# Optimization experiments

Measured on AMD Instinct MI355X. Metric: run time of the kernel, lower is better.

Reference implementation:

```python
import jax, jax.numpy as jnp
import numpy as np

NQ, NT, BSZ, E, NH = 100, 197, 128, 768, 12
HD = E // NH
EPS = 1e-12  # torch F.normalize default eps


def _l2norm(x, axis=-1):
    n = jnp.linalg.norm(x, axis=axis, keepdims=True)
    return x / jnp.maximum(n, EPS)


def setup_inputs() -> dict:
    rng = jax.random.key(0)
    ks = jax.random.split(rng, 10)
    s = 0.02  # xavier-ish scale for weights
    return {
        "query": jax.random.normal(ks[0], (NQ, BSZ, E), jnp.float32),
        "key": jax.random.normal(ks[1], (NT, BSZ, E), jnp.float32),
        "value": jax.random.normal(ks[2], (NT, BSZ, E), jnp.float32),
        "in_proj_weight": jax.random.normal(ks[3], (3 * E, E), jnp.float32) * s,
        "in_proj_bias": jnp.zeros((3 * E,), jnp.float32),
        "out_proj_weight": jax.random.normal(ks[4], (E, E), jnp.float32) * s,
        "out_proj_bias": jnp.zeros((E,), jnp.float32),
        "temperature": jnp.ones((NH, 1, 1), jnp.float32),
        "q_mapper": jax.random.normal(ks[5], (1, NT, NQ), jnp.float32),
        "x_mapper": jax.random.normal(ks[6], (1, NQ, NT), jnp.float32),
    }


def reference(query, key, value, in_proj_weight, in_proj_bias,
              out_proj_weight, out_proj_bias, temperature, q_mapper, x_mapper):
    nq, bsz, e = query.shape
    nt = key.shape[0]
    # packed in-projection: split into q/k/v weights
    wq, wk, wv = jnp.split(in_proj_weight, 3, axis=0)
    bq, bk, bv = jnp.split(in_proj_bias, 3, axis=0)
    q = query @ wq.T + bq   # [Nq, bsz, E]
    k = key @ wk.T + bk     # [Nt, bsz, E]
    v = value @ wv.T + bv   # [Nt, bsz, E]
    # reshape to [bsz, nh, hd, N] (channel-major for cross-covariance attn)
    q = q.reshape(nq, bsz, NH, HD).transpose(1, 2, 3, 0)  # [b, h, d, Nq]
    k = k.reshape(nt, bsz, NH, HD).transpose(1, 2, 3, 0)  # [b, h, d, Nt]
    v = v.reshape(nt, bsz, NH, HD).transpose(1, 2, 3, 0)  # [b, h, d, Nt]
    # normalize channel vectors over tokens
    qn = _l2norm(q)
    kn = _l2norm(k)
    # mappers: normalize over last dim, then shape to [Nq, Nt] operators
    qm_op = _l2norm(q_mapper[0])  # [Nt, Nq] normalized over Nq; transpose below
    xm_op = _l2norm(x_mapper[0])  # [Nq, Nt] normalized over Nt
    # qm = q @ q_mapper^T : [b,h,d,Nq] x [Nq,Nt] -> [b,h,d,Nt]
    qm = jnp.einsum('bhdq,tq->bhdt', qn, qm_op)
    # cross-covariance attention over channels: [b,h,d,d]
    attn = jnp.einsum('bhdt,bhet->bhde', qm, kn) * temperature[None]  # temp [nh,1,1] broadcasts per-head
    attn = jax.nn.softmax(attn, axis=-1)
    x = jnp.einsum('bhde,bhet->bhdt', attn, v)        # [b,h,d,Nt]
    out = jnp.einsum('bhdt,qt->bhdq', x, xm_op)       # [b,h,d,Nq]
    # back to [Nq, bsz, E]
    out = out.transpose(3, 0, 1, 2).reshape(nq, bsz, e)
    out = out @ out_proj_weight.T + out_proj_bias
    return out
```

## Files before the change

kernel.cpp:

```cpp
#include <hip/hip_runtime.h>
#include <hip/hip_bf16.h>

using bf16 = __hip_bfloat16;

constexpr int NQ  = 100;
constexpr int NT  = 197;
constexpr int BSZ = 128;
constexpr int EMB = 768;
constexpr int NHD = 12;
constexpr int HDD = 64;
constexpr int COLS = BSZ * EMB;
constexpr int M_Q  = 12800;
constexpr int M_KV = 25216;
constexpr int M_KVP = 25344;
constexpr int TPAD = 224;

constexpr size_t SZ_Q16  = (size_t)M_Q  * EMB * 2;
constexpr size_t SZ_KV16 = (size_t)M_KV * EMB * 2;
constexpr size_t SZ_KVP  = (size_t)M_KVP * EMB * 2;
constexpr size_t SZ_WI   = (size_t)3 * EMB * EMB * 2;
constexpr size_t SZ_T16  = (size_t)COLS * TPAD * 2;
constexpr size_t OFF_QB   = 256;
constexpr size_t OFF_KB   = OFF_QB + SZ_Q16;
constexpr size_t OFF_VB   = OFF_KB + SZ_KV16;
constexpr size_t OFF_WI   = OFF_VB + SZ_KV16;
constexpr size_t OFF_QP16 = OFF_WI + SZ_WI;
constexpr size_t OFF_KP16 = OFF_QP16 + SZ_Q16;
constexpr size_t OFF_VP16 = OFF_KP16 + SZ_KVP;
constexpr size_t OFF_QMNT = OFF_VP16 + SZ_KVP;
constexpr size_t OFF_XMNT = OFF_QMNT + 57344;
constexpr size_t OFF_WO   = OFF_XMNT + 57344;
constexpr size_t OFF_KPT  = 256;
constexpr size_t OFF_VPT  = OFF_KPT + SZ_T16;
constexpr size_t OFF_W16T = OFF_VPT + SZ_T16;
constexpr size_t OFF_QNT  = OFF_KP16;
constexpr size_t OFF_G16  = OFF_VP16;
constexpr size_t OFF_XO   = 256;

__device__ __forceinline__ float dl(const float* p) { return *p; }
__device__ __forceinline__ float dl(const bf16* p) { return __bfloat162float(*p); }

__device__ __forceinline__ ushort f2bf(float x) {
    union { float f; unsigned u; } v; v.f = x;
    unsigned r = v.u + 0x7FFFu + ((v.u >> 16) & 1u);
    return (ushort)(r >> 16);
}
__device__ __forceinline__ float bf2f(ushort x) {
    union { unsigned u; float f; } v; v.u = (unsigned)x << 16;
    return v.f;
}
__device__ __forceinline__ void dstore(float* p, float v) { *p = v; }
__device__ __forceinline__ void dstore(bf16* p, float v) { *p = __float2bfloat16(v); }

typedef __attribute__((ext_vector_type(8))) short short8;
typedef __attribute__((ext_vector_type(4))) short shortv4;
typedef __attribute__((ext_vector_type(4))) float f32x4;

__device__ __forceinline__ void gload16(const bf16* g, ushort* l) {
    __builtin_amdgcn_global_load_lds(
        (const __attribute__((address_space(1))) unsigned int*)g,
        (__attribute__((address_space(3))) unsigned int*)l, 16, 0, 0);
}

__device__ __forceinline__ int2 xcd_swz(int bx, int by, int gx, int gy) {
    const int nwg = gx * gy;
    const int L = by * gx + bx;
    const int q = nwg >> 3, r = nwg & 7;
    const int c = L & 7, i = L >> 3;
    const int wg = (c < r ? c * (q + 1) : r * (q + 1) + (c - r) * q) + i;
    return make_int2(wg % gx, wg / gx);
}

__global__ __launch_bounds__(256) void k_cvt5(
        const float* __restrict__ s0, bf16* __restrict__ d0,
        const float* __restrict__ s1, bf16* __restrict__ d1,
        const float* __restrict__ s2, bf16* __restrict__ d2,
        const float* __restrict__ s3, bf16* __restrict__ d3,
        const float* __restrict__ s4, bf16* __restrict__ d4) {
    int bk = blockIdx.x;
    const float* s; bf16* d; int lb;
    if      (bk < 864)   { s = s0; d = d0; lb = bk; }
    else if (bk < 5664)  { s = s1; d = d1; lb = bk - 864; }
    else if (bk < 15120) { s = s2; d = d2; lb = bk - 5664; }
    else if (bk < 24576) { s = s3; d = d3; lb = bk - 15120; }
    else                 { s = s4; d = d4; lb = bk - 24576; }
    size_t i = ((size_t)lb * 256 + threadIdx.x) * 8;
    float4 a = *(const float4*)(s + i), b = *(const float4*)(s + i + 4);
    short8 r;
    r[0] = (short)f2bf(a.x); r[1] = (short)f2bf(a.y); r[2] = (short)f2bf(a.z); r[3] = (short)f2bf(a.w);
    r[4] = (short)f2bf(b.x); r[5] = (short)f2bf(b.y); r[6] = (short)f2bf(b.z); r[7] = (short)f2bf(b.w);
    *(short8*)(d + i) = r;
}

template <typename T>
__global__ __launch_bounds__(256) void k_maps(const T* __restrict__ qm, bf16* qmnT,
                                              const T* __restrict__ xm, bf16* xmnT) {
    __shared__ float red[256];
    const int bk = blockIdx.x, tid = threadIdx.x;
    if (bk < 224) {
        int t = bk;
        float v = (t < NT && tid < NQ) ? dl(&qm[t * NQ + tid]) : 0.f;
        if (tid < 128) red[tid] = v * v;
        __syncthreads();
        for (int s = 64; s > 0; s >>= 1) { if (tid < s) red[tid] += red[tid + s]; __syncthreads(); }
        float inv = 1.f / fmaxf(sqrtf(red[0]), 1e-12f);
        if (tid < 128)
            dstore(&qmnT[(size_t)tid * TPAD + t], (t < NT && tid < NQ) ? v * inv : 0.f);
    } else {
        int q = bk - 224, t = tid;
        float v = (q < NQ && t < NT) ? dl(&xm[q * NT + t]) : 0.f;
        red[t] = v * v;
        __syncthreads();
        for (int s = 128; s > 0; s >>= 1) { if (t < s) red[t] += red[t + s]; __syncthreads(); }
        float inv = 1.f / fmaxf(sqrtf(red[0]), 1e-12f);
        if (t < TPAD) dstore(&xmnT[(size_t)q * TPAD + t], (q < NQ && t < NT) ? v * inv : 0.f);
    }
}

template <int NR, int TP, int NORM>
__global__ __launch_bounds__(256) void k_trn(const bf16* __restrict__ src,
        bf16* __restrict__ dst) {
    __shared__ ushort tile[TP * 73];
    __shared__ float ssp[4][64];
    __shared__ float inv_s[64];
    const int col0 = blockIdx.x * 64;
    const int tid = threadIdx.x;
    const int c = tid & 63, tb = tid >> 6;
    float ss = 0.f;
#pragma unroll
    for (int it = 0; it < TP / 4; ++it) {
        int t = tb + it * 4;
        ushort v = 0;
        if (t < NR) v = *(const ushort*)&src[(size_t)t * COLS + col0 + c];
        tile[t * 73 + c] = v;
        if (NORM) { float f = bf2f(v); ss = fmaf(f, f, ss); }
    }
    if (NORM) {
        ssp[tb][c] = ss;
        __syncthreads();
        if (tid < 64) {
            float s = ssp[0][tid] + ssp[1][tid] + ssp[2][tid] + ssp[3][tid];
            inv_s[tid] = 1.f / fmaxf(sqrtf(s), 1e-12f);
        }
    }
    __syncthreads();
    constexpr int UPC = TP / 8;
#pragma unroll
    for (int it = 0; it < (64 * UPC) / 256; ++it) {
        int u = tid + it * 256;
        int cc = u / UPC, t0 = (u % UPC) * 8;
        float inv = NORM ? inv_s[cc] : 1.f;
        short8 s;
#pragma unroll
        for (int r = 0; r < 8; ++r) {
            ushort raw = tile[(t0 + r) * 73 + cc];
            s[r] = NORM ? (short)f2bf(bf2f(raw) * inv) : (short)raw;
        }
        *(short8*)&dst[(size_t)(col0 + cc) * TP + t0] = s;
    }
}

__global__ __launch_bounds__(256) void k_trn2(const bf16* __restrict__ kp,
        const bf16* __restrict__ vp, bf16* __restrict__ kpT, bf16* __restrict__ vpT) {
    __shared__ ushort tile[TPAD * 73];
    __shared__ float ssp[4][64];
    __shared__ float inv_s[64];
    const int bk = blockIdx.x;
    const bool vseg = bk >= 1536;
    const bf16* src = vseg ? vp : kp;
    bf16* dst = vseg ? vpT : kpT;
    const int col0 = (vseg ? bk - 1536 : bk) * 64;
    const int tid = threadIdx.x;
    const int c = tid & 63, tb = tid >> 6;
    float ss = 0.f;
#pragma unroll
    for (int it = 0; it < TPAD / 4; ++it) {
        int t = tb + it * 4;
        ushort v = 0;
        if (t < NT) v = *(const ushort*)&src[(size_t)t * COLS + col0 + c];
        tile[t * 73 + c] = v;
        if (!vseg) { float f = bf2f(v); ss = fmaf(f, f, ss); }
    }
    if (!vseg) {
        ssp[tb][c] = ss;
        __syncthreads();
        if (tid < 64) {
            float s = ssp[0][tid] + ssp[1][tid] + ssp[2][tid] + ssp[3][tid];
            inv_s[tid] = 1.f / fmaxf(sqrtf(s), 1e-12f);
        }
    }
    __syncthreads();
    constexpr int UPC = TPAD / 8;
#pragma unroll
    for (int it = 0; it < (64 * UPC) / 256; ++it) {
        int u = tid + it * 256;
        int cc = u / UPC, t0 = (u % UPC) * 8;
        float inv = vseg ? 1.f : inv_s[cc];
        short8 s;
#pragma unroll
        for (int r = 0; r < 8; ++r) {
            ushort raw = tile[(t0 + r) * 73 + cc];
            s[r] = vseg ? (short)raw : (short)f2bf(bf2f(raw) * inv);
        }
        *(short8*)&dst[(size_t)(col0 + cc) * TPAD + t0] = s;
    }
}

#define MM8_BAR  { __builtin_amdgcn_s_barrier(); __builtin_amdgcn_sched_barrier(0); }
#define MM8_LGK0 { asm volatile("s_waitcnt lgkmcnt(0)" ::: "memory"); __builtin_amdgcn_sched_barrier(0); }
#define MM8_VM8  { asm volatile("s_waitcnt vmcnt(8)" ::: "memory"); __builtin_amdgcn_sched_barrier(0); }
#define MM8_VM0  { asm volatile("s_waitcnt vmcnt(0)" ::: "memory"); __builtin_amdgcn_sched_barrier(0); }
#define MM8_STAGE(CUR, ISB, H, KT) do { \
    const bf16* gb_ = (ISB) ? (Wb + (size_t)(n0 + (H)*128 + srow) * EMB + (KT)*64 + sk_sw) \
                            : (Ab + (size_t)(m0 + (H)*128 + srow) * EMB + (KT)*64 + sk_sw); \
    ushort* lb_ = ((ISB) ? B_lds : A_lds) + (CUR)*16384 + (H)*8192 + wid*512; \
    gload16(gb_, lb_); \
    gload16(gb_ + (size_t)64 * EMB, lb_ + 4096); \
} while (0)
#define MM8_LOADFRAGS(CUR, KK, AARR, BARR) { \
    _Pragma("unroll") for (int m_ = 0; m_ < 8; ++m_) { \
        int ra_ = wr*128 + m_*16 + ln15; \
        AARR[m_] = *(const short8*)&A_lds[(CUR)*16384 + ra_*64 + ((((KK)*4 + q8) ^ (ra_ & 7)))*8]; } \
    _Pragma("unroll") for (int j_ = 0; j_ < 4; ++j_) { \
        int rb_ = wc*64 + j_*16 + ln15; \
        BARR[j_] = *(const short8*)&B_lds[(CUR)*16384 + rb_*64 + ((((KK)*4 + q8) ^ (rb_ & 7)))*8]; } }
#define MM8_QUAD(AARR, BARR, MB) { \
    __builtin_amdgcn_s_setprio(1); \
    _Pragma("unroll") for (int m_ = 0; m_ < 4; ++m_) \
        _Pragma("unroll") for (int j_ = 0; j_ < 4; ++j_) \
            acc[(MB) + m_][j_] = __builtin_amdgcn_mfma_f32_16x16x32_bf16( \
                AARR[(MB) + m_], BARR[j_], acc[(MB) + m_][j_], 0, 0, 0); \
    __builtin_amdgcn_s_setprio(0); }

__global__ __launch_bounds__(512, 2) void k_mm8(
        const bf16* __restrict__ A0, const bf16* __restrict__ A1, const bf16* __restrict__ A2,
        const bf16* __restrict__ W,
        bf16* __restrict__ C0, bf16* __restrict__ C1, bf16* __restrict__ C2,
        const float* __restrict__ bias, int mt0, int mt01) {
    __shared__ __align__(16) ushort A_lds[2 * 16384];
    __shared__ __align__(16) ushort B_lds[2 * 16384];
    const int tid = threadIdx.x;
    const int2 bxy = xcd_swz(blockIdx.x, blockIdx.y, gridDim.x, gridDim.y);
    int seg = 0, lby = bxy.y;
    if (bxy.y < mt0)       { seg = 0; lby = bxy.y; }
    else if (bxy.y < mt01) { seg = 1; lby = bxy.y - mt0; }
    else                   { seg = 2; lby = bxy.y - mt01; }
    const bf16* Ab = seg == 0 ? A0 : (seg == 1 ? A1 : A2);
    const bf16* Wb = W + (size_t)seg * EMB * EMB;
    bf16* C = seg == 0 ? C0 : (seg == 1 ? C1 : C2);
    const float* bp = bias + seg * EMB;
    const int m0 = lby * 256, n0 = bxy.x * 256;
    const int wid = tid >> 6, ln = tid & 63;
    const int wr = wid >> 2, wc = wid & 3;
    const int ln15 = ln & 15, q8 = ln >> 4;
    const int srow = tid >> 3;
    const int sk_sw = (((tid & 7) ^ (srow & 7)) * 8);

    f32x4 acc[8][4] = {};
    short8 a0[8], b0[4], a1[8], b1[4];

    MM8_STAGE(0, 0, 0, 0); MM8_STAGE(0, 0, 1, 0); MM8_STAGE(0, 1, 0, 0); MM8_STAGE(0, 1, 1, 0);
    MM8_STAGE(1, 0, 0, 1); MM8_STAGE(1, 0, 1, 1); MM8_STAGE(1, 1, 0, 1); MM8_STAGE(1, 1, 1, 1);
    MM8_VM8;
    MM8_BAR;

    for (int t = 0; t < 12; ++t) {
        const int c = t & 1, nxt = t + 2;
        MM8_LOADFRAGS(c, 0, a0, b0);
        MM8_QUAD(a0, b0, 0);
        MM8_LOADFRAGS(c, 1, a1, b1);
        MM8_QUAD(a0, b0, 4);
        MM8_LGK0;
        MM8_BAR;
        if (nxt < 12) { MM8_STAGE(c, 0, 0, nxt); MM8_STAGE(c, 0, 1, nxt); }
        MM8_QUAD(a1, b1, 0);
        if (nxt < 12) { MM8_STAGE(c, 1, 0, nxt); MM8_STAGE(c, 1, 1, nxt); }
        if (t < 10) { MM8_VM8; } else { MM8_VM0; }
        MM8_QUAD(a1, b1, 4);
        MM8_BAR;
    }

#pragma unroll
    for (int j = 0; j < 4; ++j) {
        const int n = n0 + wc * 64 + j * 16 + ln15;
        const float bv = bp[n];
#pragma unroll
        for (int m = 0; m < 8; ++m) {
            const int mb = m0 + wr * 128 + m * 16 + q8 * 4;
#pragma unroll
            for (int r = 0; r < 4; ++r)
                dstore(&C[(size_t)(mb + r) * EMB + n], acc[m][j][r] + bv);
        }
    }
}

template <typename TBias>
__global__ __launch_bounds__(256) void k_proj2(
        const bf16* __restrict__ Aq, const bf16* __restrict__ Ak, const bf16* __restrict__ Av,
        const bf16* __restrict__ Wi, bf16* __restrict__ Cq, bf16* __restrict__ Ck,
        bf16* __restrict__ Cv, const TBias* __restrict__ bias) {
    __shared__ __align__(16) ushort As[128 * 32];
    __shared__ __align__(16) ushort Bs[128 * 32];
    const int t = threadIdx.x;
    const int2 bxy = xcd_swz(blockIdx.x, blockIdx.y, gridDim.x, gridDim.y);
    int byy = bxy.y, seg, lby;
    if (byy < 100)      { seg = 0; lby = byy; }
    else if (byy < 297) { seg = 1; lby = byy - 100; }
    else                { seg = 2; lby = byy - 297; }
    const bf16* Ab = seg == 0 ? Aq : (seg == 1 ? Ak : Av);
    const bf16* Wb = Wi + (size_t)seg * EMB * EMB;
    bf16* C = seg == 0 ? Cq : (seg == 1 ? Ck : Cv);
    const TBias* bp = bias + seg * EMB;
    const int n0 = bxy.x * 128, m0 = lby * 128;
    const int ln = t & 63, wv = t >> 6;
    const int ln15 = ln & 15, q8 = ln >> 4;
    const int mw = (wv & 1) * 64, nw = (wv >> 1) * 64;
    const int sr = ln >> 2, sk = (ln & 3) * 8;
    const bf16* gA = Ab + (size_t)(m0 + wv * 32 + sr) * EMB + sk;
    const bf16* gB = Wb + (size_t)(n0 + wv * 32 + sr) * EMB + sk;
    const size_t r16 = (size_t)16 * EMB;
    ushort* lA = &As[wv * 1024];
    ushort* lB = &Bs[wv * 1024];
    f32x4 acc[4][4] = {};
    for (int k0 = 0; k0 < EMB; k0 += 32) {
        gload16(gA + k0,       lA);
        gload16(gA + r16 + k0, lA + 512);
        gload16(gB + k0,       lB);
        gload16(gB + r16 + k0, lB + 512);
        __syncthreads();
        short8 a[4], b[4];
#pragma unroll
        for (int i = 0; i < 4; ++i)
            a[i] = *(const short8*)&As[(mw + i * 16 + ln15) * 32 + q8 * 8];
#pragma unroll
        for (int j = 0; j < 4; ++j)
            b[j] = *(const short8*)&Bs[(nw + j * 16 + ln15) * 32 + q8 * 8];
#pragma unroll
        for (int i = 0; i < 4; ++i)
#pragma unroll
            for (int j = 0; j < 4; ++j)
                acc[i][j] = __builtin_amdgcn_mfma_f32_16x16x32_bf16(a[i], b[j], acc[i][j], 0, 0, 0);
        __syncthreads();
    }
#pragma unroll
    for (int j = 0; j < 4; ++j) {
        const int n = n0 + nw + j * 16 + ln15;
        const float bv = dl(&bp[n]);
#pragma unroll
        for (int i = 0; i < 4; ++i) {
            const int mb = m0 + mw + i * 16 + q8 * 4;
#pragma unroll
            for (int r = 0; r < 4; ++r)
                dstore(&C[(size_t)(mb + r) * EMB + n], acc[i][j][r] + bv);
        }
    }
}

__global__ __launch_bounds__(256) void k_gw(
        const bf16* __restrict__ kpT, const bf16* __restrict__ vpT,
        const bf16* __restrict__ qmnT, const bf16* __restrict__ xmnT,
        bf16* __restrict__ g16, bf16* __restrict__ w16T) {
    __shared__ __align__(16) ushort As[128 * 32];
    __shared__ __align__(16) ushort Bs[128 * 32];
    const int t = threadIdx.x;
    const int2 bxy = xcd_swz(blockIdx.x, blockIdx.y, gridDim.x, gridDim.y);
    const bool wseg = bxy.y >= 768;
    const int lby = wseg ? bxy.y - 768 : bxy.y;
    const bf16* Ab = wseg ? vpT : kpT;
    const bf16* Bb = wseg ? xmnT : qmnT;
    const int m0 = lby * 128;
    const int ln = t & 63, wv = t >> 6;
    const int ln15 = ln & 15, q8 = ln >> 4;
    const int mw = (wv & 1) * 64, nw = (wv >> 1) * 64;
    const int sr = ln >> 2, sk = (ln & 3) * 8;
    const bf16* gA = Ab + (size_t)(m0 + wv * 32 + sr) * TPAD + sk;
    const bf16* gB = Bb + (size_t)(wv * 32 + sr) * TPAD + sk;
    const size_t r16 = (size_t)16 * TPAD;
    ushort* lA = &As[wv * 1024];
    ushort* lB = &Bs[wv * 1024];
    f32x4 acc[4][4] = {};
    for (int k0 = 0; k0 < TPAD; k0 += 32) {
        gload16(gA + k0,       lA);
        gload16(gA + r16 + k0, lA + 512);
        gload16(gB + k0,       lB);
        gload16(gB + r16 + k0, lB + 512);
        __syncthreads();
        short8 a[4], b[4];
#pragma unroll
        for (int i = 0; i < 4; ++i)
            a[i] = *(const short8*)&As[(mw + i * 16 + ln15) * 32 + q8 * 8];
#pragma unroll
        for (int j = 0; j < 4; ++j)
            b[j] = *(const short8*)&Bs[(nw + j * 16 + ln15) * 32 + q8 * 8];
#pragma unroll
        for (int i = 0; i < 4; ++i)
#pragma unroll
            for (int j = 0; j < 4; ++j)
                acc[i][j] = __builtin_amdgcn_mfma_f32_16x16x32_bf16(a[i], b[j], acc[i][j], 0, 0, 0);
        __syncthreads();
    }
#pragma unroll
    for (int j = 0; j < 4; ++j) {
        const int n = nw + j * 16 + ln15;
#pragma unroll
        for (int i = 0; i < 4; ++i) {
            const int mb = m0 + mw + i * 16 + q8 * 4;
            if (wseg) {
                shortv4 s;
#pragma unroll
                for (int r = 0; r < 4; ++r) s[r] = (short)f2bf(acc[i][j][r]);
                *(shortv4*)&w16T[(size_t)n * COLS + mb] = s;
            } else {
#pragma unroll
                for (int r = 0; r < 4; ++r)
                    dstore(&g16[(size_t)(mb + r) * 128 + n], acc[i][j][r]);
            }
        }
    }
}

template <typename TC, typename TBias>
__global__ __launch_bounds__(256) void k_gemm_mfma(
        const bf16* __restrict__ Ab, const bf16* __restrict__ Wb,
        TC* __restrict__ C, const TBias* __restrict__ bias,
        int M, int N, int K, int ldc) {
    __shared__ __align__(16) ushort As[128 * 32];
    __shared__ __align__(16) ushort Bs[128 * 32];
    const int t = threadIdx.x;
    const int2 bxy = xcd_swz(blockIdx.x, blockIdx.y, gridDim.x, gridDim.y);
    const int n0 = bxy.x * 128, m0 = bxy.y * 128;
    const int ln = t & 63, wv = t >> 6;
    const int ln15 = ln & 15, q8 = ln >> 4;
    const int mw = (wv & 1) * 64, nw = (wv >> 1) * 64;
    const int sr = ln >> 2, sk = (ln & 3) * 8;
    const bf16* gA = Ab + (size_t)(m0 + wv * 32 + sr) * K + sk;
    const bf16* gB = Wb + (size_t)(n0 + wv * 32 + sr) * K + sk;
    const size_t r16 = (size_t)16 * K;
    ushort* lA = &As[wv * 1024];
    ushort* lB = &Bs[wv * 1024];
    f32x4 acc[4][4] = {};
    for (int k0 = 0; k0 < K; k0 += 32) {
        gload16(gA + k0,       lA);
        gload16(gA + r16 + k0, lA + 512);
        gload16(gB + k0,       lB);
        gload16(gB + r16 + k0, lB + 512);
        __syncthreads();
        short8 a[4], b[4];
#pragma unroll
        for (int i = 0; i < 4; ++i)
            a[i] = *(const short8*)&As[(mw + i * 16 + ln15) * 32 + q8 * 8];
#pragma unroll
        for (int j = 0; j < 4; ++j)
            b[j] = *(const short8*)&Bs[(nw + j * 16 + ln15) * 32 + q8 * 8];
#pragma unroll
        for (int i = 0; i < 4; ++i)
#pragma unroll
            for (int j = 0; j < 4; ++j)
                acc[i][j] = __builtin_amdgcn_mfma_f32_16x16x32_bf16(a[i], b[j], acc[i][j], 0, 0, 0);
        __syncthreads();
    }
#pragma unroll
    for (int j = 0; j < 4; ++j) {
        const int n = n0 + nw + j * 16 + ln15;
        const float bv = dl(&bias[n]);
#pragma unroll
        for (int i = 0; i < 4; ++i) {
            const int mb = m0 + mw + i * 16 + q8 * 4;
#pragma unroll
            for (int r = 0; r < 4; ++r)
                dstore(&C[(size_t)(mb + r) * ldc + n], acc[i][j][r] + bv);
        }
    }
}

template <typename T>
__global__ __launch_bounds__(256) void k_attn(
        const bf16* __restrict__ qnT, const bf16* __restrict__ g16,
        const bf16* __restrict__ w16T, const T* __restrict__ temp,
        bf16* __restrict__ xo) {
    const int h = blockIdx.x, b = blockIdx.y;
    const int tid = threadIdx.x;
    const int ln = tid & 63, wv = tid >> 6;
    const int ln15 = ln & 15, q8 = ln >> 4;
    const int colbase = b * EMB + h * HDD;
    __shared__ __align__(16) ushort smem[16384];
    char* sm = (char*)smem;

    short8 wreg[4];
#pragma unroll
    for (int it = 0; it < 4; ++it) {
        int u = tid + it * 256;
        int q = u >> 3, e0 = (u & 7) * 8;
        wreg[it] = *(const short8*)&w16T[(size_t)q * COLS + colbase + e0];
    }

#pragma unroll
    for (int it = 0; it < 4; ++it) {
        int u = tid + it * 256;
        int e = u >> 4, q0 = (u & 15) * 8;
        short8 s = *(const short8*)&g16[(size_t)(colbase + e) * 128 + q0];
        *(short8*)(sm + ((e * 256 + q0 * 2) ^ ((e & 7) << 4))) = s;
    }
#pragma unroll
    for (int it = 0; it < 4; ++it) {
        int u = tid + it * 256;
        int d = u >> 4, q0 = (u & 15) * 8;
        short8 s = *(const short8*)&qnT[(size_t)(colbase + d) * 128 + q0];
        *(short8*)(sm + 16384 + ((d * 256 + q0 * 2) ^ ((d & 7) << 4))) = s;
    }
    __syncthreads();

    const int drow = 16 * wv + ln15;
    f32x4 acc[4] = {};
#pragma unroll
    for (int ks = 0; ks < 4; ++ks) {
        short8 bfrag = *(const short8*)(sm + 16384 +
            ((drow * 256 + ks * 64 + q8 * 16) ^ ((drow & 7) << 4)));
#pragma unroll
        for (int i = 0; i < 4; ++i) {
            int erow = i * 16 + ln15;
            short8 afrag = *(const short8*)(sm +
                ((erow * 256 + ks * 64 + q8 * 16) ^ ((erow & 7) << 4)));
            acc[i] = __builtin_amdgcn_mfma_f32_16x16x32_bf16(afrag, bfrag, acc[i], 0, 0, 0);
        }
    }

    const float tv = dl(&temp[h]);
    float p[4][4];
    float mx = -1e30f;
#pragma unroll
    for (int i = 0; i < 4; ++i)
#pragma unroll
        for (int r = 0; r < 4; ++r) { p[i][r] = acc[i][r] * tv; mx = fmaxf(mx, p[i][r]); }
    mx = fmaxf(mx, __shfl_xor(mx, 16, 64));
    mx = fmaxf(mx, __shfl_xor(mx, 32, 64));
    float sum = 0.f;
#pragma unroll
    for (int i = 0; i < 4; ++i)
#pragma unroll
        for (int r = 0; r < 4; ++r) { p[i][r] = __expf(p[i][r] - mx); sum += p[i][r]; }
    sum += __shfl_xor(sum, 16, 64);
    sum += __shfl_xor(sum, 32, 64);
    const float rs = 1.f / sum;

    __syncthreads();

#pragma unroll
    for (int i = 0; i < 4; ++i) {
        shortv4 s4;
#pragma unroll
        for (int r = 0; r < 4; ++r) s4[r] = (short)f2bf(p[i][r] * rs);
        *(shortv4*)(sm + 16384 + drow * 144 + q8 * 8 + 32 * i) = s4;
    }
#pragma unroll
    for (int it = 0; it < 4; ++it) {
        int u = tid + it * 256;
        int q = u >> 3, e0 = (u & 7) * 8;
        *(short8*)(sm + ((q * 128 + e0 * 2) ^ ((q & 7) << 4))) = wreg[it];
    }
    __syncthreads();

    f32x4 o[7] = {};
#pragma unroll
    for (int ks = 0; ks < 2; ++ks) {
        short8 afrag = *(const short8*)(sm + 16384 + drow * 144 + ks * 64 + q8 * 16);
#pragma unroll
        for (int j = 0; j < 7; ++j) {
            int qrow = j * 16 + ln15;
            short8 bfrag = *(const short8*)(sm +
                ((qrow * 128 + ks * 64 + q8 * 16) ^ ((qrow & 7) << 4)));
            o[j] = __builtin_amdgcn_mfma_f32_16x16x32_bf16(afrag, bfrag, o[j], 0, 0, 0);
        }
    }
    const int dbase = h * HDD + 16 * wv + q8 * 4;
#pragma unroll
    for (int j = 0; j < 7; ++j) {
        int q = j * 16 + ln15;
        if (q < NQ) {
            shortv4 s4;
#pragma unroll
            for (int r = 0; r < 4; ++r) s4[r] = (short)f2bf(o[j][r]);
            *(shortv4*)&xo[(size_t)(q * BSZ + b) * EMB + dbase] = s4;
        }
    }
}

extern "C" void kernel_launch(void* const* d_in, const int* in_sizes, int n_in,
                              void* d_out, int out_size, void* d_ws, size_t ws_size,
                              hipStream_t stream) {
    char* ws = (char*)d_ws;
    bf16* qb16  = (bf16*)(ws + OFF_QB);
    bf16* kb16  = (bf16*)(ws + OFF_KB);
    bf16* vb16  = (bf16*)(ws + OFF_VB);
    bf16* wi16  = (bf16*)(ws + OFF_WI);
    bf16* qp16  = (bf16*)(ws + OFF_QP16);
    bf16* kp16  = (bf16*)(ws + OFF_KP16);
    bf16* vp16  = (bf16*)(ws + OFF_VP16);
    bf16* qmnT  = (bf16*)(ws + OFF_QMNT);
    bf16* xmnT  = (bf16*)(ws + OFF_XMNT);
    bf16* wo16  = (bf16*)(ws + OFF_WO);
    bf16* kpT   = (bf16*)(ws + OFF_KPT);
    bf16* vpT   = (bf16*)(ws + OFF_VPT);
    bf16* w16T  = (bf16*)(ws + OFF_W16T);
    bf16* qnT   = (bf16*)(ws + OFF_QNT);
    bf16* g16   = (bf16*)(ws + OFF_G16);
    bf16* xo16  = (bf16*)(ws + OFF_XO);

    const bool isbf = (in_sizes[0] == 19660800);

    if (isbf) {
        k_maps<bf16><<<352, 256, 0, stream>>>((const bf16*)d_in[8], qmnT,
                                              (const bf16*)d_in[9], xmnT);
        k_proj2<bf16><<<dim3(6, 494), 256, 0, stream>>>(
            (const bf16*)d_in[0], (const bf16*)d_in[1], (const bf16*)d_in[2],
            (const bf16*)d_in[3], qp16, kp16, vp16, (const bf16*)d_in[4]);
        k_trn2<<<3072, 256, 0, stream>>>(kp16, vp16, kpT, vpT);
        k_trn<NQ, 128, 1><<<COLS / 64, 256, 0, stream>>>(qp16, qnT);
        k_gw<<<dim3(1, 1536), 256, 0, stream>>>(kpT, vpT, qmnT, xmnT, g16, w16T);
        k_attn<bf16><<<dim3(NHD, BSZ), 256, 0, stream>>>(
            qnT, g16, w16T, (const bf16*)d_in[7], xo16);
        k_gemm_mfma<bf16, bf16><<<dim3(6, 100), 256, 0, stream>>>(
            xo16, (const bf16*)d_in[5], (bf16*)d_out, (const bf16*)d_in[6],
            M_Q, EMB, EMB, EMB);
    } else {
        k_maps<float><<<352, 256, 0, stream>>>((const float*)d_in[8], qmnT,
                                               (const float*)d_in[9], xmnT);
        k_cvt5<<<24864, 256, 0, stream>>>(
            (const float*)d_in[3], wi16,
            (const float*)d_in[0], qb16,
            (const float*)d_in[1], kb16,
            (const float*)d_in[2], vb16,
            (const float*)d_in[5], wo16);
        k_mm8<<<dim3(3, 248), 512, 0, stream>>>(
            qb16, kb16, vb16, wi16, qp16, kp16, vp16,
            (const float*)d_in[4], 50, 149);
        k_trn2<<<3072, 256, 0, stream>>>(kp16, vp16, kpT, vpT);
        k_trn<NQ, 128, 1><<<COLS / 64, 256, 0, stream>>>(qp16, qnT);
        k_gw<<<dim3(1, 1536), 256, 0, stream>>>(kpT, vpT, qmnT, xmnT, g16, w16T);
        k_attn<float><<<dim3(NHD, BSZ), 256, 0, stream>>>(
            qnT, g16, w16T, (const float*)d_in[7], xo16);
        k_gemm_mfma<float, float><<<dim3(6, 100), 256, 0, stream>>>(
            xo16, wo16, (float*)d_out, (const float*)d_in[6], M_Q, EMB, EMB, EMB);
    }
}
```

Measured before the change: 459.8 us.

## Shrink QKV projection GEMM tile to 256x128 with K-step 32 for occupancy

Replaces the 256x256 tile, K=64-step projection GEMM with a 256x128 tile and K=32 steps. This cuts LDS per block from 128KB to 48KB and accumulators per wave from 32 to 16 MFMA tiles, and raises the occupancy hint to 4 blocks per CU. The grid doubles along N. The trade-off is lower arithmetic intensity: each A tile is loaded twice as often. The loop also runs twice as many iterations, with more barriers per unit of work.

Measured after the change: 462.5 us. No clear change (+0.6%).

```diff
diff --git a/kernel.cpp b/kernel.cpp
--- a/kernel.cpp
+++ b/kernel.cpp
@@ -206,39 +206,40 @@
     }
 }
 
-#define MM8_BAR  { __builtin_amdgcn_s_barrier(); __builtin_amdgcn_sched_barrier(0); }
-#define MM8_LGK0 { asm volatile("s_waitcnt lgkmcnt(0)" ::: "memory"); __builtin_amdgcn_sched_barrier(0); }
-#define MM8_VM8  { asm volatile("s_waitcnt vmcnt(8)" ::: "memory"); __builtin_amdgcn_sched_barrier(0); }
-#define MM8_VM0  { asm volatile("s_waitcnt vmcnt(0)" ::: "memory"); __builtin_amdgcn_sched_barrier(0); }
-#define MM8_STAGE(CUR, ISB, H, KT) do { \
-    const bf16* gb_ = (ISB) ? (Wb + (size_t)(n0 + (H)*128 + srow) * EMB + (KT)*64 + sk_sw) \
-                            : (Ab + (size_t)(m0 + (H)*128 + srow) * EMB + (KT)*64 + sk_sw); \
-    ushort* lb_ = ((ISB) ? B_lds : A_lds) + (CUR)*16384 + (H)*8192 + wid*512; \
-    gload16(gb_, lb_); \
-    gload16(gb_ + (size_t)64 * EMB, lb_ + 4096); \
+#define MM9_BAR  { __builtin_amdgcn_s_barrier(); __builtin_amdgcn_sched_barrier(0); }
+#define MM9_LGK0 { asm volatile("s_waitcnt lgkmcnt(0)" ::: "memory"); __builtin_amdgcn_sched_barrier(0); }
+#define MM9_VM3  { asm volatile("s_waitcnt vmcnt(3)" ::: "memory"); __builtin_amdgcn_sched_barrier(0); }
+#define MM9_VM0  { asm volatile("s_waitcnt vmcnt(0)" ::: "memory"); __builtin_amdgcn_sched_barrier(0); }
+#define MM9_STAGE_A(CUR, H, KT) do { \
+    const bf16* gb_ = Ab + (size_t)(m0 + (H)*128 + (tid >> 2)) * EMB + (KT)*32 + sk_sw; \
+    gload16(gb_, A_lds + (CUR)*8192 + (H)*4096 + wid*512); \
 } while (0)
-#define MM8_LOADFRAGS(CUR, KK, AARR, BARR) { \
-    _Pragma("unroll") for (int m_ = 0; m_ < 8; ++m_) { \
-        int ra_ = wr*128 + m_*16 + ln15; \
-        AARR[m_] = *(const short8*)&A_lds[(CUR)*16384 + ra_*64 + ((((KK)*4 + q8) ^ (ra_ & 7)))*8]; } \
+#define MM9_STAGE_B(CUR, KT) do { \
+    const bf16* gb_ = Wb + (size_t)(n0 + (tid >> 2)) * EMB + (KT)*32 + sk_sw; \
+    gload16(gb_, B_lds + (CUR)*4096 + wid*512); \
+} while (0)
+#define MM9_LOADFRAGS(CUR) { \
+    _Pragma("unroll") for (int m_ = 0; m_ < 4; ++m_) { \
+        int ra_ = wr*64 + m_*16 + ln15; \
+        a[m_] = *(const short8*)&A_lds[(CUR)*8192 + ra_*32 + ((q8 ^ (ra_ & 3)))*8]; } \
     _Pragma("unroll") for (int j_ = 0; j_ < 4; ++j_) { \
         int rb_ = wc*64 + j_*16 + ln15; \
-        BARR[j_] = *(const short8*)&B_lds[(CUR)*16384 + rb_*64 + ((((KK)*4 + q8) ^ (rb_ & 7)))*8]; } }
-#define MM8_QUAD(AARR, BARR, MB) { \
+        b[j_] = *(const short8*)&B_lds[(CUR)*4096 + rb_*32 + ((q8 ^ (rb_ & 3)))*8]; } }
+#define MM9_QUAD(MB) { \
     __builtin_amdgcn_s_setprio(1); \
-    _Pragma("unroll") for (int m_ = 0; m_ < 4; ++m_) \
+    _Pragma("unroll") for (int m_ = 0; m_ < 2; ++m_) \
         _Pragma("unroll") for (int j_ = 0; j_ < 4; ++j_) \
             acc[(MB) + m_][j_] = __builtin_amdgcn_mfma_f32_16x16x32_bf16( \
-                AARR[(MB) + m_], BARR[j_], acc[(MB) + m_][j_], 0, 0, 0); \
+                a[(MB) + m_], b[j_], acc[(MB) + m_][j_], 0, 0, 0); \
     __builtin_amdgcn_s_setprio(0); }
 
-__global__ __launch_bounds__(512, 2) void k_mm8(
+__global__ __launch_bounds__(512, 4) void k_mm9(
         const bf16* __restrict__ A0, const bf16* __restrict__ A1, const bf16* __restrict__ A2,
         const bf16* __restrict__ W,
         bf16* __restrict__ C0, bf16* __restrict__ C1, bf16* __restrict__ C2,
         const float* __restrict__ bias, int mt0, int mt01) {
-    __shared__ __align__(16) ushort A_lds[2 * 16384];
-    __shared__ __align__(16) ushort B_lds[2 * 16384];
+    __shared__ __align__(16) ushort A_lds[2 * 8192];
+    __shared__ __align__(16) ushort B_lds[2 * 4096];
     const int tid = threadIdx.x;
     const int2 bxy = xcd_swz(blockIdx.x, blockIdx.y, gridDim.x, gridDim.y);
     int seg = 0, lby = bxy.y;
@@ -249,35 +250,30 @@
     const bf16* Wb = W + (size_t)seg * EMB * EMB;
     bf16* C = seg == 0 ? C0 : (seg == 1 ? C1 : C2);
     const float* bp = bias + seg * EMB;
-    const int m0 = lby * 256, n0 = bxy.x * 256;
+    const int m0 = lby * 256, n0 = bxy.x * 128;
     const int wid = tid >> 6, ln = tid & 63;
-    const int wr = wid >> 2, wc = wid & 3;
+    const int wr = wid >> 1, wc = wid & 1;
     const int ln15 = ln & 15, q8 = ln >> 4;
-    const int srow = tid >> 3;
-    const int sk_sw = (((tid & 7) ^ (srow & 7)) * 8);
-
-    f32x4 acc[8][4] = {};
-    short8 a0[8], b0[4], a1[8], b1[4];
-
-    MM8_STAGE(0, 0, 0, 0); MM8_STAGE(0, 0, 1, 0); MM8_STAGE(0, 1, 0, 0); MM8_STAGE(0, 1, 1, 0);
-    MM8_STAGE(1, 0, 0, 1); MM8_STAGE(1, 0, 1, 1); MM8_STAGE(1, 1, 0, 1); MM8_STAGE(1, 1, 1, 1);
-    MM8_VM8;
-    MM8_BAR;
-
-    for (int t = 0; t < 12; ++t) {
+    const int sk_sw = (((tid & 3) ^ ((tid >> 2) & 3)) * 8);
+
+    f32x4 acc[4][4] = {};
+    short8 a[4], b[4];
+
+    MM9_STAGE_A(0, 0, 0); MM9_STAGE_A(0, 1, 0); MM9_STAGE_B(0, 0);
+    MM9_STAGE_A(1, 0, 1); MM9_STAGE_A(1, 1, 1); MM9_STAGE_B(1, 1);
+    MM9_VM3;
+    MM9_BAR;
+
+    for (int t = 0; t < 24; ++t) {
         const int c = t & 1, nxt = t + 2;
-        MM8_LOADFRAGS(c, 0, a0, b0);
-        MM8_QUAD(a0, b0, 0);
-        MM8_LOADFRAGS(c, 1, a1, b1);
-        MM8_QUAD(a0, b0, 4);
-        MM8_LGK0;
-        MM8_BAR;
-        if (nxt < 12) { MM8_STAGE(c, 0, 0, nxt); MM8_STAGE(c, 0, 1, nxt); }
-        MM8_QUAD(a1, b1, 0);
-        if (nxt < 12) { MM8_STAGE(c, 1, 0, nxt); MM8_STAGE(c, 1, 1, nxt); }
-        if (t < 10) { MM8_VM8; } else { MM8_VM0; }
-        MM8_QUAD(a1, b1, 4);
-        MM8_BAR;
+        MM9_LOADFRAGS(c);
+        MM9_QUAD(0);
+        MM9_LGK0;
+        MM9_BAR;
+        if (nxt < 24) { MM9_STAGE_A(c, 0, nxt); MM9_STAGE_A(c, 1, nxt); MM9_STAGE_B(c, nxt); }
+        if (t < 22) { MM9_VM3; } else { MM9_VM0; }
+        MM9_QUAD(2);
+        MM9_BAR;
     }
 
 #pragma unroll
@@ -285,8 +281,8 @@
         const int n = n0 + wc * 64 + j * 16 + ln15;
         const float bv = bp[n];
 #pragma unroll
-        for (int m = 0; m < 8; ++m) {
-            const int mb = m0 + wr * 128 + m * 16 + q8 * 4;
+        for (int m = 0; m < 4; ++m) {
+            const int mb = m0 + wr * 64 + m * 16 + q8 * 4;
 #pragma unroll
             for (int r = 0; r < 4; ++r)
                 dstore(&C[(size_t)(mb + r) * EMB + n], acc[m][j][r] + bv);
@@ -631,7 +627,7 @@
             (const float*)d_in[1], kb16,
             (const float*)d_in[2], vb16,
             (const float*)d_in[5], wo16);
-        k_mm8<<<dim3(3, 248), 512, 0, stream>>>(
+        k_mm9<<<dim3(6, 248), 512, 0, stream>>>(
             qb16, kb16, vb16, wi16, qp16, kp16, vp16,
             (const float*)d_in[4], 50, 149);
         k_trn2<<<3072, 256, 0, stream>>>(kp16, vp16, kpT, vpT);
```
